# Optimization experiments

Hardware: AMD Instinct MI355X
Metric: run time of the kernel (lower is better)

The kernel has to match this reference:

```python
import jax, jax.numpy as jnp
import numpy as np

D_MODEL = 1024
NUM_HEADS = 16

def _dense_params(key, d_in, d_out):
    kw, _ = jax.random.split(key)
    # flax default: lecun_normal kernel, zeros bias
    W = jax.random.normal(kw, (d_in, d_out), dtype=jnp.float32) / np.sqrt(d_in)
    b = jnp.zeros((d_out,), dtype=jnp.float32)
    return W, b

def setup_inputs() -> dict:
    key = jax.random.key(0)
    ks = jax.random.split(key, 8)
    B, Tx, Tc = 2, 2048, 2048
    x = jax.random.normal(ks[0], (B, Tx, D_MODEL), dtype=jnp.float32)
    context = jax.random.normal(ks[1], (B, Tc, D_MODEL), dtype=jnp.float32)
    Wq, bq = _dense_params(ks[2], D_MODEL, D_MODEL)
    Wks, bks = _dense_params(ks[3], D_MODEL, D_MODEL)
    Wvs, bvs = _dense_params(ks[4], D_MODEL, D_MODEL)
    Wkc, bkc = _dense_params(ks[5], D_MODEL, D_MODEL)
    Wvc, bvc = _dense_params(ks[6], D_MODEL, D_MODEL)
    Wo, bo = _dense_params(ks[7], D_MODEL, D_MODEL)
    return {"x": x, "context": context,
            "Wq": Wq, "bq": bq, "Wks": Wks, "bks": bks, "Wvs": Wvs, "bvs": bvs,
            "Wkc": Wkc, "bkc": bkc, "Wvc": Wvc, "bvc": bvc, "Wo": Wo, "bo": bo}

def _split_heads(t, H):
    B, T, C = t.shape
    return t.reshape(B, T, H, C // H).transpose(0, 2, 1, 3)  # [B,H,T,hd]

def reference(x, context, Wq, bq, Wks, bks, Wvs, bvs, Wkc, bkc, Wvc, bvc, Wo, bo):
    H = NUM_HEADS
    head_dim = D_MODEL // H
    q = x @ Wq + bq
    k = jnp.concatenate([x @ Wks + bks, context @ Wkc + bkc], axis=1)
    v = jnp.concatenate([x @ Wvs + bvs, context @ Wvc + bvc], axis=1)
    q = _split_heads(q, H)  # [B,H,Tq,hd]
    k = _split_heads(k, H)  # [B,H,Tk,hd]
    v = _split_heads(v, H)
    attn = jnp.einsum('bhqd,bhkd->bhqk', q, k) / jnp.sqrt(jnp.float32(head_dim))
    attn = jax.nn.softmax(attn, axis=-1)
    out = jnp.einsum('bhqk,bhkd->bhqd', attn, v)
    B, _, Tq, _ = out.shape
    out = out.transpose(0, 2, 1, 3).reshape(B, Tq, D_MODEL)
    return out @ Wo + bo
```

## Files before the change

kernel.cpp:

```cpp
#include <hip/hip_runtime.h>
#include <hip/hip_bf16.h>
#include <math.h>


typedef _Float16 f16;
typedef _Float16 f16x8 __attribute__((ext_vector_type(8)));
typedef _Float16 f16x4v __attribute__((ext_vector_type(4)));
typedef _Float16 f16x2 __attribute__((ext_vector_type(2)));
typedef float    f32x4 __attribute__((ext_vector_type(4)));
typedef float    f32x16 __attribute__((ext_vector_type(16)));
typedef unsigned u32x4v __attribute__((ext_vector_type(4)));

#define MFMA_F16(a, b, c)  __builtin_amdgcn_mfma_f32_16x16x32_f16((a), (b), (c), 0, 0, 0)
#define MFMA32_F16(a, b, c) __builtin_amdgcn_mfma_f32_32x32x16_f16((a), (b), (c), 0, 0, 0)

#define QSCALE 0.18033688011112042f

__device__ __forceinline__ void glds16(const f16* g, f16* l) {
    __builtin_amdgcn_global_load_lds(
        (const __attribute__((address_space(1))) void*)g,
        (__attribute__((address_space(3))) void*)l, 16, 0, 0);
}

__device__ __forceinline__ unsigned pk16(float a, float b) {
    f16x2 t = { (f16)a, (f16)b };
    return __builtin_bit_cast(unsigned, t);
}

__global__ __launch_bounds__(256) void prep(
    const float4* __restrict__ x, const float4* __restrict__ ctx,
    f16x4v* __restrict__ xb, f16x4v* __restrict__ cb,
    const float* __restrict__ W0, const float* __restrict__ W1,
    const float* __restrict__ W2, const float* __restrict__ W3,
    const float* __restrict__ W4, const float* __restrict__ W5,
    f16* __restrict__ wt)
{
    if (blockIdx.x < 8192) {
        const int n4 = (2 * 2048 * 1024) / 4;
        int i = blockIdx.x * 256 + threadIdx.x;
        float4 v;
        f16x4v* dst;
        if (i < n4) { v = x[i];        dst = xb + i; }
        else        { v = ctx[i - n4]; dst = cb + (i - n4); }
        f16x4v h = { (f16)v.x, (f16)v.y, (f16)v.z, (f16)v.w };
        *dst = h;
        return;
    }
    const int idx = blockIdx.x - 8192;
    const int z = idx >> 10, rem = idx & 1023;
    const float* Ws[6] = { W0, W1, W2, W3, W4, W5 };
    const float* W = Ws[z];
    f16* Wt = wt + (size_t)z * (1024 * 1024);

    __shared__ float tile[32][33];
    const int tx = threadIdx.x & 31, ty = threadIdx.x >> 5;
    const int n0 = (rem & 31) * 32, k0 = (rem >> 5) * 32;

#pragma unroll
    for (int i = 0; i < 4; ++i) {
        int r = i * 8 + ty;
        tile[r][tx] = W[(size_t)(k0 + r) * 1024 + n0 + tx];
    }
    __syncthreads();
#pragma unroll
    for (int i = 0; i < 4; ++i) {
        int r = i * 8 + ty;
        Wt[(size_t)(n0 + r) * 1024 + k0 + tx] = (f16)tile[tx][r];
    }
}

#define GEMM_PROLOGUE(BN)                                                     \
    const int m0 = blockIdx.x * 128, n0 = blockIdx.y * (BN);                  \
    const int tid = threadIdx.x;                                              \
    const int w = tid >> 6, lane = tid & 63, quad = lane >> 4, l15 = lane & 15;\
    const int wm = (w >> 1) * 64, wn = (w & 1) * ((BN) / 2);                  \
    const int qsw = (quad ^ ((l15 >> 1) & 3)) * 8;                            \
    int gA[2], gB[(BN) / 64];                                                 \
    _Pragma("unroll")                                                         \
    for (int p = 0; p < 2; ++p) {                                             \
        int s = tid + p * 256;                                                \
        int r = (s >> 2) & 127, c = (s & 3) ^ ((s >> 3) & 3);                 \
        gA[p] = (m0 + r) * 1024 + c * 8;                                      \
    }                                                                         \
    _Pragma("unroll")                                                         \
    for (int p = 0; p < (BN) / 64; ++p) {                                     \
        int s = tid + p * 256;                                                \
        int r = (s >> 2) & ((BN) - 1), c = (s & 3) ^ ((s >> 3) & 3);          \
        gB[p] = (n0 + r) * 1024 + c * 8;                                      \
    }

#define GEMM_STAGE_TO(BN, buf, koff)                                          \
    _Pragma("unroll")                                                         \
    for (int p = 0; p < 2; ++p)                                               \
        glds16(&A[gA[p] + (koff)], &As[buf][(p * 256 + w * 64) * 8]);         \
    _Pragma("unroll")                                                         \
    for (int p = 0; p < (BN) / 64; ++p)                                       \
        glds16(&Bt[gB[p] + (koff)], &Bs[buf][(p * 256 + w * 64) * 8]);

__global__ __launch_bounds__(256) void proj_gemm(
    const f16* __restrict__ xb, const f16* __restrict__ cb,
    const f16* __restrict__ wt,
    const float* __restrict__ bq, const float* __restrict__ bks,
    const float* __restrict__ bkc, const float* __restrict__ bvs,
    const float* __restrict__ bvc,
    f16* __restrict__ qbuf, f16* __restrict__ kbuf, f16* __restrict__ vbuf)
{
    __shared__ alignas(16) f16 As[3][128 * 32];
    __shared__ alignas(16) f16 Bs[3][128 * 32];

    const int z = blockIdx.z;
    const f16* A = (z == 0 || z == 1 || z == 3) ? xb : cb;
    const int wslot = (z == 0) ? 0 : (z == 1) ? 1 : (z == 2) ? 3 : (z == 3) ? 2 : 4;
    const f16* Bt = wt + (size_t)wslot * 1048576;
    const float* bias = (z == 0) ? bq : (z == 1) ? bks : (z == 2) ? bkc
                        : (z == 3) ? bvs : bvc;
    const int roff = (z == 2 || z == 4) ? 2048 : 0;

    GEMM_PROLOGUE(128)
    f32x4 acc[4][4] = {};

    GEMM_STAGE_TO(128, 0, 0)
    GEMM_STAGE_TO(128, 1, 32)

    for (int it = 0; it < 32; ++it) {
        if (it < 31) { asm volatile("s_waitcnt vmcnt(4)" ::: "memory"); }
        else         { asm volatile("s_waitcnt vmcnt(0)" ::: "memory"); }
        __builtin_amdgcn_s_barrier();
        if (it + 2 < 32) {
            GEMM_STAGE_TO(128, (it + 2) % 3, (it + 2) * 32)
        }
        const f16* Asc = As[it % 3];
        const f16* Bsc = Bs[it % 3];
        f16x8 a[4], b[4];
#pragma unroll
        for (int i = 0; i < 4; ++i)
            a[i] = *(const f16x8*)&Asc[(wm + i * 16 + l15) * 32 + qsw];
#pragma unroll
        for (int i = 0; i < 4; ++i)
            b[i] = *(const f16x8*)&Bsc[(wn + i * 16 + l15) * 32 + qsw];
#pragma unroll
        for (int mi = 0; mi < 4; ++mi)
#pragma unroll
            for (int ni = 0; ni < 4; ++ni)
                acc[mi][ni] = MFMA_F16(a[mi], b[ni], acc[mi][ni]);
    }

#pragma unroll
    for (int mi = 0; mi < 4; ++mi) {
#pragma unroll
        for (int r = 0; r < 4; ++r) {
            int row = m0 + wm + mi * 16 + quad * 4 + r;
            int b_ = row >> 11, tok = row & 2047;
#pragma unroll
            for (int ni = 0; ni < 4; ++ni) {
                int col = n0 + wn + ni * 16 + l15;
                float v = acc[mi][ni][r] + bias[col];
                int bh = b_ * 16 + (col >> 6);
                int tg = roff + tok;
                if (z == 0) {
                    qbuf[((size_t)bh * 2048 + tok) * 64 + (col & 63)] = (f16)(v * QSCALE);
                } else if (z <= 2) {
                    kbuf[(size_t)bh * 262144 + (size_t)(tg >> 6) * 4096
                         + (size_t)((col >> 5) & 1) * 2048 + (tg & 63) * 32 + (col & 31)] = (f16)v;
                } else {
                    vbuf[(size_t)bh * 262144 + (size_t)tg * 64 + (col & 63)] = (f16)v;
                }
            }
        }
    }
}

__global__ __launch_bounds__(256) void transpose_v(
    const f16* __restrict__ vbuf, f16* __restrict__ vt)
{
    const int t = threadIdx.x;
    const int mt = t >> 3, md = t & 7;
    const int tok0 = blockIdx.x * 256 + mt * 8;
    const int z = blockIdx.y;
    f16x8 in[8];
#pragma unroll
    for (int i = 0; i < 8; ++i)
        in[i] = *(const f16x8*)&vbuf[((size_t)z * 4096 + tok0 + i) * 64 + md * 8];
    f16x8 ov[8];
#pragma unroll
    for (int j = 0; j < 8; ++j)
#pragma unroll
        for (int i = 0; i < 8; ++i) ov[j][i] = in[i][j];
    const int kt = tok0 >> 6, kks = (tok0 >> 5) & 1, kko = tok0 & 31;
#pragma unroll
    for (int j = 0; j < 8; ++j)
        *(f16x8*)&vt[(size_t)z * 262144 + (size_t)kt * 4096 + kks * 2048
                     + (md * 8 + j) * 32 + kko] = ov[j];
}

__global__ __launch_bounds__(256, 4) void attn_kernel(
    const f16* __restrict__ q, const f16* __restrict__ kb,
    const f16* __restrict__ vtb, f16* __restrict__ osplit,
    float* __restrict__ lsplit)
{
    __shared__ alignas(16) f16 K_lds[2][4096];
    __shared__ alignas(16) f16 V_lds[2][4096];

    const int tid = threadIdx.x;
    const int w = tid >> 6, lane = tid & 63;
    const int l31 = lane & 31, h = lane >> 5;
    const int bh = blockIdx.x, qt = blockIdx.y, sp = blockIdx.z;
    const int qbase = qt * 128;

    f16x8 qa[4];
    {
        const size_t qrow = ((size_t)bh * 2048 + qbase + w * 32 + l31) * 64;
#pragma unroll
        for (int kc = 0; kc < 4; ++kc)
            qa[kc] = *(const f16x8*)&q[qrow + kc * 16 + h * 8];
    }

    f32x16 o_acc[2] = {};
    float l_part = 0.f;

    const f16* ktile = kb + (size_t)bh * 262144 + (size_t)sp * 131072;
    const f16* vtile = vtb + (size_t)bh * 262144 + (size_t)sp * 131072;

    const int sco = ((tid >> 2) * 4 + ((tid & 3) ^ ((tid >> 3) & 3))) * 8;
    const int ksw = (l31 >> 1) & 3;
    const int wslot = w * 512;

    glds16(ktile + sco,        &K_lds[0][wslot]);
    glds16(ktile + 2048 + sco, &K_lds[0][2048 + wslot]);
    glds16(vtile + sco,        &V_lds[0][wslot]);
    glds16(vtile + 2048 + sco, &V_lds[0][2048 + wslot]);

    for (int kt = 0; kt < 32; ++kt) {
        const int cur = kt & 1;
        const f16* Kc = K_lds[cur];
        const f16* Vc = V_lds[cur];

        __syncthreads();

        if (kt != 31) {
            ktile += 4096; vtile += 4096;
            glds16(ktile + sco,        &K_lds[cur ^ 1][wslot]);
            glds16(ktile + 2048 + sco, &K_lds[cur ^ 1][2048 + wslot]);
            glds16(vtile + sco,        &V_lds[cur ^ 1][wslot]);
            glds16(vtile + 2048 + sco, &V_lds[cur ^ 1][2048 + wslot]);
        }

#pragma unroll
        for (int mt = 0; mt < 2; ++mt) {
            f32x16 s = {};
            __builtin_amdgcn_s_setprio(1);
#pragma unroll
            for (int kc = 0; kc < 4; ++kc) {
                f16x8 ka = *(const f16x8*)&Kc[(kc >> 1) * 2048
                             + (mt * 32 + l31) * 32
                             + ((((kc & 1) * 2 + h) ^ ksw)) * 8];
                s = MFMA32_F16(ka, qa[kc], s);
            }
            __builtin_amdgcn_s_setprio(0);

            float pe[16];
#pragma unroll
            for (int i = 0; i < 16; ++i) pe[i] = __builtin_amdgcn_exp2f(s[i]);

            {
                float t0 = (pe[0] + pe[1]) + (pe[2] + pe[3]);
                float t1 = (pe[4] + pe[5]) + (pe[6] + pe[7]);
                float t2 = (pe[8] + pe[9]) + (pe[10] + pe[11]);
                float t3 = (pe[12] + pe[13]) + (pe[14] + pe[15]);
                l_part += (t0 + t1) + (t2 + t3);
            }

#pragma unroll
            for (int c = 0; c < 2; ++c) {
                const int cb = c * 8;
                unsigned X0 = pk16(pe[cb + 0], pe[cb + 1]);
                unsigned X1 = pk16(pe[cb + 2], pe[cb + 3]);
                unsigned Y0 = pk16(pe[cb + 4], pe[cb + 5]);
                unsigned Y1 = pk16(pe[cb + 6], pe[cb + 7]);
                auto r0 = __builtin_amdgcn_permlane32_swap(X0, Y0, false, false);
                auto r1 = __builtin_amdgcn_permlane32_swap(X1, Y1, false, false);
                u32x4v pw;
                pw[0] = r0[0]; pw[1] = r1[0]; pw[2] = r0[1]; pw[3] = r1[1];
                f16x8 pfrag = __builtin_bit_cast(f16x8, pw);

                const int kchunk = mt * 2 + c;
                __builtin_amdgcn_s_setprio(1);
#pragma unroll
                for (int db = 0; db < 2; ++db) {
                    f16x8 va = *(const f16x8*)&Vc[(kchunk >> 1) * 2048
                                 + (db * 32 + l31) * 32
                                 + (((((kchunk & 1) * 2 + h)) ^ ksw)) * 8];
                    o_acc[db] = MFMA32_F16(va, pfrag, o_acc[db]);
                }
                __builtin_amdgcn_s_setprio(0);
            }
        }
    }

    float lf = l_part + __shfl_xor(l_part, 32, 64);
    float inv = 1.0f / lf;
    const int row = w * 32 + l31;
    const size_t sb = (size_t)(sp * 32 + bh) * 2048 + qbase;
    if (h == 0) lsplit[sb + row] = lf;
    const size_t obase = (sb + row) * 64;
#pragma unroll
    for (int db = 0; db < 2; ++db) {
#pragma unroll
        for (int g = 0; g < 4; ++g) {
            f16x4v ov;
#pragma unroll
            for (int i = 0; i < 4; ++i)
                ov[i] = (f16)(o_acc[db][g * 4 + i] * inv);
            *(f16x4v*)&osplit[obase + db * 32 + g * 8 + h * 4] = ov;
        }
    }
}

__global__ __launch_bounds__(256) void out_gemm(
    const f16* __restrict__ osplit, const float* __restrict__ lsplit,
    const f16* __restrict__ wt5, const float* __restrict__ bo,
    float* __restrict__ out)
{
    __shared__ alignas(16) f16 As[2][64 * 32];
    __shared__ alignas(16) f16 Bs[3][64 * 32];

    const int m0 = blockIdx.x * 64, n0 = blockIdx.y * 64;
    const int tid = threadIdx.x;
    const int w = tid >> 6, lane = tid & 63, quad = lane >> 4, l15 = lane & 15;
    const int wm = (w >> 1) * 32, wn = (w & 1) * 32;
    const int qsw = (quad ^ ((l15 >> 1) & 3)) * 8;
    const int r_ = (tid >> 2) & 63, c_ = (tid & 3) ^ ((tid >> 3) & 3);
    const int rowg = m0 + r_;
    const int b_ = rowg >> 11, tok = rowg & 2047;
    const int gB = (n0 + r_) * 1024 + c_ * 8;
    const int lslot = w * 512 + lane * 8;

    f32x4 acc[2][2] = {};

#define OA(s, it) (&osplit[(((size_t)(s) * 32 + b_ * 16 + ((it) >> 1)) * 2048 \
                            + tok) * 64 + ((it) & 1) * 32 + c_ * 8])
#define OL(s, it) ((s) * 65536 + (b_ * 16 + ((it) >> 1)) * 2048 + tok)

#define MERGE_WRITE(buf, a1, a2, l1, l2)                                      \
    {                                                                         \
        float inv_ = 1.0f / ((l1) + (l2));                                    \
        float w1_ = (l1) * inv_, w2_ = (l2) * inv_;                           \
        f16x8 m_;                                                             \
        _Pragma("unroll")                                                     \
        for (int j_ = 0; j_ < 8; ++j_)                                        \
            m_[j_] = (f16)(w1_ * (float)(a1)[j_] + w2_ * (float)(a2)[j_]);    \
        *(f16x8*)&As[buf][lslot] = m_;                                        \
    }

    glds16(&wt5[gB], &Bs[0][w * 512]);
    f16x8 a1 = *(const f16x8*)OA(0, 0);
    f16x8 a2 = *(const f16x8*)OA(1, 0);
    float l1 = lsplit[OL(0, 0)];
    float l2 = lsplit[OL(1, 0)];
    glds16(&wt5[gB + 32], &Bs[1][w * 512]);
    MERGE_WRITE(0, a1, a2, l1, l2)
    asm volatile("s_waitcnt lgkmcnt(0)" ::: "memory");
    __builtin_amdgcn_s_barrier();

    for (int it = 0; it < 32; ++it) {
        f16x8 na1, na2;
        float nl1, nl2;
        if (it < 31) {
            na1 = *(const f16x8*)OA(0, it + 1);
            na2 = *(const f16x8*)OA(1, it + 1);
            nl1 = lsplit[OL(0, it + 1)];
            nl2 = lsplit[OL(1, it + 1)];
            if (it + 2 < 32)
                glds16(&wt5[gB + (it + 2) * 32], &Bs[(it + 2) % 3][w * 512]);
        }

        const f16* Asc = As[it & 1];
        const f16* Bsc = Bs[it % 3];
        f16x8 a[2], b[2];
#pragma unroll
        for (int i = 0; i < 2; ++i)
            a[i] = *(const f16x8*)&Asc[(wm + i * 16 + l15) * 32 + qsw];
#pragma unroll
        for (int i = 0; i < 2; ++i)
            b[i] = *(const f16x8*)&Bsc[(wn + i * 16 + l15) * 32 + qsw];
#pragma unroll
        for (int mi = 0; mi < 2; ++mi)
#pragma unroll
            for (int ni = 0; ni < 2; ++ni)
                acc[mi][ni] = MFMA_F16(a[mi], b[ni], acc[mi][ni]);

        if (it < 31) {
            MERGE_WRITE((it + 1) & 1, na1, na2, nl1, nl2)
        }
        asm volatile("s_waitcnt lgkmcnt(0)" ::: "memory");
        __builtin_amdgcn_s_barrier();
    }

#pragma unroll
    for (int mi = 0; mi < 2; ++mi) {
#pragma unroll
        for (int r = 0; r < 4; ++r) {
            int row = m0 + wm + mi * 16 + quad * 4 + r;
#pragma unroll
            for (int ni = 0; ni < 2; ++ni) {
                int col = n0 + wn + ni * 16 + l15;
                out[(size_t)row * 1024 + col] = acc[mi][ni][r] + bo[col];
            }
        }
    }
#undef OA
#undef OL
#undef MERGE_WRITE
}

extern "C" void kernel_launch(void* const* d_in, const int* in_sizes, int n_in,
                              void* d_out, int out_size, void* d_ws, size_t ws_size,
                              hipStream_t stream)
{
    (void)in_sizes; (void)n_in; (void)out_size; (void)ws_size;

    const float* x    = (const float*)d_in[0];
    const float* ctx  = (const float*)d_in[1];
    const float* Wq   = (const float*)d_in[2];  const float* bq  = (const float*)d_in[3];
    const float* Wks  = (const float*)d_in[4];  const float* bks = (const float*)d_in[5];
    const float* Wvs  = (const float*)d_in[6];  const float* bvs = (const float*)d_in[7];
    const float* Wkc  = (const float*)d_in[8];  const float* bkc = (const float*)d_in[9];
    const float* Wvc  = (const float*)d_in[10]; const float* bvc = (const float*)d_in[11];
    const float* Wo   = (const float*)d_in[12]; const float* bo  = (const float*)d_in[13];

    char* ws = (char*)d_ws;
    f16*   xb     = (f16*)(ws + 0);
    f16*   cb     = (f16*)(ws + 8388608);
    f16*   vt     = (f16*)(ws + 0);
    f16*   wt     = (f16*)(ws + 16777216);
    float* lsplit = (float*)(ws + 16777216);
    f16*   qbuf   = (f16*)(ws + 29360128);
    f16*   kbuf   = (f16*)(ws + 37748736);
    f16*   vbuf   = (f16*)(ws + 54525952);
    f16*   osplit = (f16*)(ws + 54525952);

    prep<<<14336, 256, 0, stream>>>((const float4*)x, (const float4*)ctx,
                                    (f16x4v*)xb, (f16x4v*)cb,
                                    Wq, Wks, Wvs, Wkc, Wvc, Wo, wt);

    proj_gemm<<<dim3(32, 8, 5), 256, 0, stream>>>(
        xb, cb, wt, bq, bks, bkc, bvs, bvc, qbuf, kbuf, vbuf);

    transpose_v<<<dim3(16, 32), 256, 0, stream>>>(vbuf, vt);

    attn_kernel<<<dim3(32, 16, 2), 256, 0, stream>>>(qbuf, kbuf, vt, osplit, lsplit);

    out_gemm<<<dim3(64, 16), 256, 0, stream>>>(osplit, lsplit,
                                               wt + 5 * 1048576, bo, (float*)d_out);
}
```

Baseline: 307.4 us.

## Process two query groups per attention block to reuse K/V tiles

Each attention block now handles 256 query rows (two groups of 128) instead of 128, so every K/V tile loaded into LDS and every K/V fragment read into registers is reused across both groups. The grid is halved along the query dimension and the occupancy hint drops from 4 to 2 blocks per CU to make room for the doubled accumulators and Q fragments. This targets global and LDS traffic in the attention loop, at the cost of fewer blocks (512) for latency hiding and higher register pressure.

```diff
diff --git a/kernel.cpp b/kernel.cpp
--- a/kernel.cpp
+++ b/kernel.cpp
@@ -193,7 +193,7 @@
                      + (md * 8 + j) * 32 + kko] = ov[j];
 }
 
-__global__ __launch_bounds__(256, 4) void attn_kernel(
+__global__ __launch_bounds__(256, 2) void attn_kernel(
     const f16* __restrict__ q, const f16* __restrict__ kb,
     const f16* __restrict__ vtb, f16* __restrict__ osplit,
     float* __restrict__ lsplit)
@@ -205,18 +205,20 @@
     const int w = tid >> 6, lane = tid & 63;
     const int l31 = lane & 31, h = lane >> 5;
     const int bh = blockIdx.x, qt = blockIdx.y, sp = blockIdx.z;
-    const int qbase = qt * 128;
-
-    f16x8 qa[4];
-    {
-        const size_t qrow = ((size_t)bh * 2048 + qbase + w * 32 + l31) * 64;
+    const int qbase = qt * 256;
+
+    f16x8 qa[2][4];
+#pragma unroll
+    for (int grp = 0; grp < 2; ++grp) {
+        const size_t qrow =
+            ((size_t)bh * 2048 + qbase + grp * 128 + w * 32 + l31) * 64;
 #pragma unroll
         for (int kc = 0; kc < 4; ++kc)
-            qa[kc] = *(const f16x8*)&q[qrow + kc * 16 + h * 8];
-    }
-
-    f32x16 o_acc[2] = {};
-    float l_part = 0.f;
+            qa[grp][kc] = *(const f16x8*)&q[qrow + kc * 16 + h * 8];
+    }
+
+    f32x16 o_acc[2][2] = {};
+    float l_part[2] = { 0.f, 0.f };
 
     const f16* ktile = kb + (size_t)bh * 262144 + (size_t)sp * 131072;
     const f16* vtile = vtb + (size_t)bh * 262144 + (size_t)sp * 131072;
@@ -247,71 +249,85 @@
 
 #pragma unroll
         for (int mt = 0; mt < 2; ++mt) {
-            f32x16 s = {};
-            __builtin_amdgcn_s_setprio(1);
-#pragma unroll
-            for (int kc = 0; kc < 4; ++kc) {
-                f16x8 ka = *(const f16x8*)&Kc[(kc >> 1) * 2048
+            f16x8 ka[4];
+#pragma unroll
+            for (int kc = 0; kc < 4; ++kc)
+                ka[kc] = *(const f16x8*)&Kc[(kc >> 1) * 2048
                              + (mt * 32 + l31) * 32
                              + ((((kc & 1) * 2 + h) ^ ksw)) * 8];
-                s = MFMA32_F16(ka, qa[kc], s);
+            f16x8 va[2][2];
+#pragma unroll
+            for (int c = 0; c < 2; ++c)
+#pragma unroll
+                for (int db = 0; db < 2; ++db) {
+                    const int kchunk = mt * 2 + c;
+                    va[c][db] = *(const f16x8*)&Vc[(kchunk >> 1) * 2048
+                                 + (db * 32 + l31) * 32
+                                 + ((((kchunk & 1) * 2 + h) ^ ksw)) * 8];
+                }
+
+#pragma unroll
+            for (int grp = 0; grp < 2; ++grp) {
+                f32x16 s = {};
+                __builtin_amdgcn_s_setprio(1);
+#pragma unroll
+                for (int kc = 0; kc < 4; ++kc)
+                    s = MFMA32_F16(ka[kc], qa[grp][kc], s);
+                __builtin_amdgcn_s_setprio(0);
+
+                float pe[16];
+#pragma unroll
+                for (int i = 0; i < 16; ++i) pe[i] = __builtin_amdgcn_exp2f(s[i]);
+
+                {
+                    float t0 = (pe[0] + pe[1]) + (pe[2] + pe[3]);
+                    float t1 = (pe[4] + pe[5]) + (pe[6] + pe[7]);
+                    float t2 = (pe[8] + pe[9]) + (pe[10] + pe[11]);
+                    float t3 = (pe[12] + pe[13]) + (pe[14] + pe[15]);
+                    l_part[grp] += (t0 + t1) + (t2 + t3);
+                }
+
+#pragma unroll
+                for (int c = 0; c < 2; ++c) {
+                    const int cb = c * 8;
+                    unsigned X0 = pk16(pe[cb + 0], pe[cb + 1]);
+                    unsigned X1 = pk16(pe[cb + 2], pe[cb + 3]);
+                    unsigned Y0 = pk16(pe[cb + 4], pe[cb + 5]);
+                    unsigned Y1 = pk16(pe[cb + 6], pe[cb + 7]);
+                    auto r0 = __builtin_amdgcn_permlane32_swap(X0, Y0, false, false);
+                    auto r1 = __builtin_amdgcn_permlane32_swap(X1, Y1, false, false);
+                    u32x4v pw;
+                    pw[0] = r0[0]; pw[1] = r1[0]; pw[2] = r0[1]; pw[3] = r1[1];
+                    f16x8 pfrag = __builtin_bit_cast(f16x8, pw);
+
+                    __builtin_amdgcn_s_setprio(1);
+#pragma unroll
+                    for (int db = 0; db < 2; ++db)
+                        o_acc[grp][db] = MFMA32_F16(va[c][db], pfrag, o_acc[grp][db]);
+                    __builtin_amdgcn_s_setprio(0);
+                }
             }
-            __builtin_amdgcn_s_setprio(0);
-
-            float pe[16];
-#pragma unroll
-            for (int i = 0; i < 16; ++i) pe[i] = __builtin_amdgcn_exp2f(s[i]);
-
-            {
-                float t0 = (pe[0] + pe[1]) + (pe[2] + pe[3]);
-                float t1 = (pe[4] + pe[5]) + (pe[6] + pe[7]);
-                float t2 = (pe[8] + pe[9]) + (pe[10] + pe[11]);
-                float t3 = (pe[12] + pe[13]) + (pe[14] + pe[15]);
-                l_part += (t0 + t1) + (t2 + t3);
+        }
+    }
+
+    const size_t sb = (size_t)(sp * 32 + bh) * 2048 + qbase;
+#pragma unroll
+    for (int grp = 0; grp < 2; ++grp) {
+        float lf = l_part[grp] + __shfl_xor(l_part[grp], 32, 64);
+        float inv = 1.0f / lf;
+        const int rowl = grp * 128 + w * 32 + l31;
+        if (h == 0) lsplit[sb + rowl] = lf;
+        const size_t obase = (sb + rowl) * 64;
+#pragma unroll
+        for (int db = 0; db < 2; ++db) {
+#pragma unroll
+            for (int g = 0; g < 4; ++g) {
+                f16x4v ov;
+#pragma unroll
+                for (int i = 0; i < 4; ++i)
+                    ov[i] = (f16)(o_acc[grp][db][g * 4 + i] * inv);
+                *(f16x4v*)&osplit[obase + db * 32 + g * 8 + h * 4] = ov;
             }
-
-#pragma unroll
-            for (int c = 0; c < 2; ++c) {
-                const int cb = c * 8;
-                unsigned X0 = pk16(pe[cb + 0], pe[cb + 1]);
-                unsigned X1 = pk16(pe[cb + 2], pe[cb + 3]);
-                unsigned Y0 = pk16(pe[cb + 4], pe[cb + 5]);
-                unsigned Y1 = pk16(pe[cb + 6], pe[cb + 7]);
-                auto r0 = __builtin_amdgcn_permlane32_swap(X0, Y0, false, false);
-                auto r1 = __builtin_amdgcn_permlane32_swap(X1, Y1, false, false);
-                u32x4v pw;
-                pw[0] = r0[0]; pw[1] = r1[0]; pw[2] = r0[1]; pw[3] = r1[1];
-                f16x8 pfrag = __builtin_bit_cast(f16x8, pw);
-
-                const int kchunk = mt * 2 + c;
-                __builtin_amdgcn_s_setprio(1);
-#pragma unroll
-                for (int db = 0; db < 2; ++db) {
-                    f16x8 va = *(const f16x8*)&Vc[(kchunk >> 1) * 2048
-                                 + (db * 32 + l31) * 32
-                                 + (((((kchunk & 1) * 2 + h)) ^ ksw)) * 8];
-                    o_acc[db] = MFMA32_F16(va, pfrag, o_acc[db]);
-                }
-                __builtin_amdgcn_s_setprio(0);
-            }
-        }
-    }
-
-    float lf = l_part + __shfl_xor(l_part, 32, 64);
-    float inv = 1.0f / lf;
-    const int row = w * 32 + l31;
-    const size_t sb = (size_t)(sp * 32 + bh) * 2048 + qbase;
-    if (h == 0) lsplit[sb + row] = lf;
-    const size_t obase = (sb + row) * 64;
-#pragma unroll
-    for (int db = 0; db < 2; ++db) {
-#pragma unroll
-        for (int g = 0; g < 4; ++g) {
-            f16x4v ov;
-#pragma unroll
-            for (int i = 0; i < 4; ++i)
-                ov[i] = (f16)(o_acc[db][g * 4 + i] * inv);
-            *(f16x4v*)&osplit[obase + db * 32 + g * 8 + h * 4] = ov;
         }
     }
 }
@@ -448,7 +464,7 @@
 
     transpose_v<<<dim3(16, 32), 256, 0, stream>>>(vbuf, vt);
 
-    attn_kernel<<<dim3(32, 16, 2), 256, 0, stream>>>(qbuf, kbuf, vt, osplit, lsplit);
+    attn_kernel<<<dim3(32, 8, 2), 256, 0, stream>>>(qbuf, kbuf, vt, osplit, lsplit);
 
     out_gemm<<<dim3(64, 16), 256, 0, stream>>>(osplit, lsplit,
                                                wt + 5 * 1048576, bo, (float*)d_out);
```

Result: no change. 307.0 us (-0.1%).
